# Kernel tuning notes

Hardware: AMD Instinct MI355X
Metric: run time of the kernel (lower is better)

The kernel has to match this reference:

```python
import jax, jax.numpy as jnp
import numpy as np

D_MODEL = 1024
N_HEAD = 16
D_HEAD = D_MODEL // N_HEAD


def setup_inputs() -> dict:
    key = jax.random.key(0)
    k1, k2, k3 = jax.random.split(key, 3)
    x = jax.random.normal(k1, (4, 1024, D_MODEL), dtype=jnp.float32)
    # torch Linear(d_model, 3*d_model, bias=False): weight [3*d_model, d_model], y = x @ W.T
    w_qkv = jax.random.normal(k2, (3 * D_MODEL, D_MODEL), dtype=jnp.float32) * (1.0 / np.sqrt(D_MODEL))
    w_out = jax.random.normal(k3, (D_MODEL, D_MODEL), dtype=jnp.float32) * (1.0 / np.sqrt(D_MODEL))
    return {"x": x, "w_qkv": w_qkv, "w_out": w_out}


def reference(x, w_qkv, w_out):
    B, T, C = x.shape
    qkv = x @ w_qkv.T                                   # [B,T,3C]
    qkv = qkv.reshape(B, T, 3, N_HEAD, D_HEAD)
    q = jnp.transpose(qkv[:, :, 0], (0, 2, 1, 3))       # [B,H,T,Dh]
    k = jnp.transpose(qkv[:, :, 1], (0, 2, 1, 3))
    v = jnp.transpose(qkv[:, :, 2], (0, 2, 1, 3))
    att = jnp.einsum('bhqd,bhkd->bhqk', q, k) / jnp.sqrt(jnp.float32(D_HEAD))
    causal = jnp.tril(jnp.ones((T, T), dtype=bool))
    att = jnp.where(causal[None, None], att, -jnp.inf)
    att = jax.nn.softmax(att, axis=-1)
    y = jnp.einsum('bhqk,bhkd->bhqd', att, v)           # [B,H,T,Dh]
    y = jnp.transpose(y, (0, 2, 1, 3)).reshape(B, T, C)
    return y @ w_out.T
```

## Files before the change

kernel.cpp:

```cpp
#include <hip/hip_runtime.h>
#include <hip/hip_bf16.h>
#include <stdint.h>

#define DM 1024
#define NH 16
#define DH 64
#define BB 4
#define TT 1024
#define MR (BB*TT)

typedef __attribute__((ext_vector_type(8))) short bf16x8;
typedef __attribute__((ext_vector_type(4))) float f32x4;

typedef unsigned int __attribute__((address_space(1))) uint_g;
typedef unsigned int __attribute__((address_space(3))) uint_l;

static __device__ __forceinline__ void gload_lds16(const void* g, void* l) {
  __builtin_amdgcn_global_load_lds((const uint_g*)g, (uint_l*)l, 16, 0, 0);
}

static __device__ __forceinline__ unsigned short f2bf(float f) {
  union { float f; unsigned int u; } v; v.f = f;
  unsigned int r = v.u + 0x7fffu + ((v.u >> 16) & 1u);
  return (unsigned short)(r >> 16);
}
static __device__ __forceinline__ unsigned short f2bf_fast(float f) {
  union { float f; unsigned int u; } v; v.f = f;
  return (unsigned short)((v.u + 0x8000u) >> 16);
}

__global__ __launch_bounds__(256) void k_cvt3(const float* __restrict__ x,
    const float* __restrict__ w1, const float* __restrict__ w2,
    unsigned short* __restrict__ xb, unsigned short* __restrict__ wqb,
    unsigned short* __restrict__ wob) {
  const int n1 = (MR * DM) / 4, n2 = (3 * DM * DM) / 4, n3 = (DM * DM) / 4;
  const int total = n1 + n2 + n3;
  for (int u = blockIdx.x * 256 + threadIdx.x; u < total; u += gridDim.x * 256) {
    const float* src; unsigned short* dst; int i;
    if (u < n1)           { src = x;  dst = xb;  i = u; }
    else if (u < n1 + n2) { src = w1; dst = wqb; i = u - n1; }
    else                  { src = w2; dst = wob; i = u - n1 - n2; }
    float4 v = reinterpret_cast<const float4*>(src)[i];
    ushort4 o;
    o.x = f2bf(v.x); o.y = f2bf(v.y); o.z = f2bf(v.z); o.w = f2bf(v.w);
    reinterpret_cast<ushort4*>(dst)[i] = o;
  }
}

template<int EPI>
__global__ __launch_bounds__(256) void k_gemm(
    const unsigned short* __restrict__ A, const unsigned short* __restrict__ Bw,
    float* __restrict__ Of, unsigned short* __restrict__ qb,
    unsigned short* __restrict__ kb, unsigned short* __restrict__ vtb,
    int N, int K, int tiles_n) {
  __shared__ unsigned short SH[2][2][128 * 32];
  int tid = threadIdx.x;
  int w = tid >> 6, l = tid & 63;
  int l15 = l & 15, k8 = l >> 4;
  int nwg = gridDim.x;
  int cpx = nwg >> 3;
  int wg = blockIdx.x;
  int swz = (wg & 7) * cpx + (wg >> 3);
  int tm = swz / tiles_n, tn = swz % tiles_n;
  int m0 = tm << 7, n0 = tn << 7;

  f32x4 acc[4][4];
  #pragma unroll
  for (int i = 0; i < 4; ++i)
    #pragma unroll
    for (int j = 0; j < 4; ++j) acc[i][j] = (f32x4){0.f, 0.f, 0.f, 0.f};

  int srow = (w << 4) + (l >> 2);
  int sch = l & 3;
  int mrb = ((w >> 1) << 6) + l15;
  int nrb = ((w & 1) << 6) + l15;

  auto stage = [&](int buf, int kk) {
    #pragma unroll
    for (int p = 0; p < 2; ++p) {
      int row = srow + (p << 6);
      int c = sch ^ ((row >> 1) & 3);
      int seg = w + (p << 2);
      gload_lds16(A + (size_t)(m0 + row) * K + kk + (c << 3), &SH[buf][0][seg << 9]);
      gload_lds16(Bw + (size_t)(n0 + row) * K + kk + (c << 3), &SH[buf][1][seg << 9]);
    }
  };

  stage(0, 0);
  __syncthreads();
  int cur = 0;
  for (int kk = 0; kk < K; kk += 32) {
    if (kk + 32 < K) stage(cur ^ 1, kk + 32);
    bf16x8 a[4], b[4];
    #pragma unroll
    for (int mf = 0; mf < 4; ++mf) {
      int row = mrb + (mf << 4);
      a[mf] = *(const bf16x8*)&SH[cur][0][(row << 5) + ((k8 ^ ((row >> 1) & 3)) << 3)];
    }
    #pragma unroll
    for (int nf = 0; nf < 4; ++nf) {
      int row = nrb + (nf << 4);
      b[nf] = *(const bf16x8*)&SH[cur][1][(row << 5) + ((k8 ^ ((row >> 1) & 3)) << 3)];
    }
    #pragma unroll
    for (int mf = 0; mf < 4; ++mf)
      #pragma unroll
      for (int nf = 0; nf < 4; ++nf)
        acc[mf][nf] = __builtin_amdgcn_mfma_f32_16x16x32_bf16(a[mf], b[nf], acc[mf][nf], 0, 0, 0);
    __syncthreads();
    cur ^= 1;
  }

  if (EPI == 1) {
    #pragma unroll
    for (int mf = 0; mf < 4; ++mf)
      #pragma unroll
      for (int nf = 0; nf < 4; ++nf) {
        int n = n0 + ((w & 1) << 6) + (nf << 4) + l15;
        int m_base = m0 + ((w >> 1) << 6) + (mf << 4) + (k8 << 2);
        #pragma unroll
        for (int r = 0; r < 4; ++r)
          Of[(size_t)(m_base + r) * N + n] = acc[mf][nf][r];
      }
    return;
  }

  int s = n0 >> 10;
  if (s < 2) {
    #pragma unroll
    for (int mf = 0; mf < 4; ++mf) {
      #pragma unroll
      for (int nf = 0; nf < 4; ++nf) {
        int n = n0 + ((w & 1) << 6) + (nf << 4) + l15;
        int rem = n & 1023;
        int h = rem >> 6, d = rem & 63;
        int m_base = m0 + ((w >> 1) << 6) + (mf << 4) + (k8 << 2);
        #pragma unroll
        for (int r = 0; r < 4; ++r) {
          int m = m_base + r;
          int bb = m >> 10, t = m & 1023;
          float v = acc[mf][nf][r];
          if (s == 0)
            qb[((size_t)(bb * NH + h) * TT + t) * DH + d] = f2bf(v * 0.125f);
          else
            kb[((size_t)(bb * NH + h) * TT + t) * DH + d] = f2bf(v);
        }
      }
    }
  } else {
    unsigned short* T = &SH[0][0][0];
    int bb = m0 >> 10, t0 = m0 & 1023;
    int myhalf = w & 1;
    #pragma unroll
    for (int half = 0; half < 2; ++half) {
      __syncthreads();
      if (myhalf == half) {
        #pragma unroll
        for (int nf = 0; nf < 4; ++nf) {
          int nloc = (nf << 4) + l15;
          #pragma unroll
          for (int mf = 0; mf < 4; ++mf) {
            int mloc = ((w >> 1) << 6) + (mf << 4) + (k8 << 2);
            #pragma unroll
            for (int r = 0; r < 4; ++r)
              T[nloc * 134 + mloc + r] = f2bf(acc[mf][nf][r]);
          }
        }
      }
      __syncthreads();
      {
        int d = tid >> 2, mseg = tid & 3;
        int n = n0 + (half << 6) + d;
        int h = (n & 1023) >> 6;
        size_t base = ((size_t)(bb * NH + h) * DH + d) * TT + t0 + (mseg << 5);
        #pragma unroll
        for (int i = 0; i < 4; ++i) {
          ushort4 v4 = *(const ushort4*)&T[d * 134 + (mseg << 5) + (i << 3)];
          ushort4 v4b = *(const ushort4*)&T[d * 134 + (mseg << 5) + (i << 3) + 4];
          *(ushort4*)&vtb[base + (i << 3)] = v4;
          *(ushort4*)&vtb[base + (i << 3) + 4] = v4b;
        }
      }
    }
  }
}

__global__ __launch_bounds__(256) void k_gemm1(
    const unsigned short* __restrict__ A, const unsigned short* __restrict__ Bw,
    float* __restrict__ Of, int N, int K) {
  __shared__ unsigned short At[2][64 * 32];
  __shared__ unsigned short Bt[2][128 * 32];
  int tid = threadIdx.x;
  int w = tid >> 6, l = tid & 63;
  int l15 = l & 15, k8 = l >> 4;
  int wg = blockIdx.x;
  int swz = (wg & 7) * 64 + (wg >> 3);
  int tm = swz >> 3, tn = swz & 7;
  int m0 = tm << 6, n0 = tn << 7;
  int wm = w >> 1, wn = w & 1;

  f32x4 acc[2][4];
  #pragma unroll
  for (int i = 0; i < 2; ++i)
    #pragma unroll
    for (int j = 0; j < 4; ++j) acc[i][j] = (f32x4){0.f, 0.f, 0.f, 0.f};

  int srl = l >> 2;
  int sch = l & 3;

  auto stage = [&](int buf, int kk) {
    {
      int row = (w << 4) + srl;
      int c = sch ^ ((row >> 1) & 3);
      gload_lds16(A + (size_t)(m0 + row) * K + kk + (c << 3), &At[buf][w << 9]);
    }
    #pragma unroll
    for (int p = 0; p < 2; ++p) {
      int seg = (w << 1) + p;
      int row = (seg << 4) + srl;
      int c = sch ^ ((row >> 1) & 3);
      gload_lds16(Bw + (size_t)(n0 + row) * K + kk + (c << 3), &Bt[buf][seg << 9]);
    }
  };

  stage(0, 0);
  __syncthreads();
  int cur = 0;
  for (int kk = 0; kk < K; kk += 32) {
    if (kk + 32 < K) stage(cur ^ 1, kk + 32);
    bf16x8 a[2], b[4];
    #pragma unroll
    for (int mf = 0; mf < 2; ++mf) {
      int row = (wm << 5) + (mf << 4) + l15;
      a[mf] = *(const bf16x8*)&At[cur][(row << 5) + ((k8 ^ ((row >> 1) & 3)) << 3)];
    }
    #pragma unroll
    for (int nf = 0; nf < 4; ++nf) {
      int row = (wn << 6) + (nf << 4) + l15;
      b[nf] = *(const bf16x8*)&Bt[cur][(row << 5) + ((k8 ^ ((row >> 1) & 3)) << 3)];
    }
    #pragma unroll
    for (int mf = 0; mf < 2; ++mf)
      #pragma unroll
      for (int nf = 0; nf < 4; ++nf)
        acc[mf][nf] = __builtin_amdgcn_mfma_f32_16x16x32_bf16(a[mf], b[nf], acc[mf][nf], 0, 0, 0);
    __syncthreads();
    cur ^= 1;
  }

  #pragma unroll
  for (int mf = 0; mf < 2; ++mf)
    #pragma unroll
    for (int nf = 0; nf < 4; ++nf) {
      int n = n0 + (wn << 6) + (nf << 4) + l15;
      int m_base = m0 + (wm << 5) + (mf << 4) + (k8 << 2);
      #pragma unroll
      for (int r = 0; r < 4; ++r)
        Of[(size_t)(m_base + r) * N + n] = acc[mf][nf][r];
    }
}

__global__ __launch_bounds__(512) void k_attn(
    const unsigned short* __restrict__ qb, const unsigned short* __restrict__ kb,
    const unsigned short* __restrict__ vtb, unsigned short* __restrict__ yb) {
  __shared__ unsigned short Kt[2][64 * 64];
  __shared__ unsigned short Vt[2][64 * 64];
  __shared__ unsigned short Pl[8][16][72];
  int tid = threadIdx.x, w = tid >> 6, l = tid & 63;
  int l15 = l & 15, k8 = l >> 4;
  int bh = blockIdx.x >> 3;
  int a = blockIdx.x & 7;
  int wlo = w & 3;
  int qb_w = (w < 4) ? ((a << 6) + (wlo << 4))
                     : ((TT - ((a + 1) << 6)) + (wlo << 4));
  const unsigned short* Kb = kb + (size_t)bh * TT * DH;
  const unsigned short* Vb = vtb + (size_t)bh * DH * TT;
  const unsigned short* Qb = qb + (size_t)bh * TT * DH;

  int qrow = qb_w + l15;
  bf16x8 qf[2];
  #pragma unroll
  for (int c = 0; c < 2; ++c)
    qf[c] = *(const bf16x8*)&Qb[(size_t)qrow * DH + (c << 5) + (k8 << 3)];

  f32x4 y[4];
  #pragma unroll
  for (int i = 0; i < 4; ++i) y[i] = (f32x4){0.f, 0.f, 0.f, 0.f};
  float mrow = -INFINITY, lrow = 0.f;

  int srow = l >> 3;
  int sch = l & 7;

  auto stage = [&](int buf, int j0) {
    int row = (w << 3) + srow;
    int c = sch ^ (row & 7);
    gload_lds16(Kb + (size_t)(j0 + row) * DH + (c << 3), &Kt[buf][(w << 3) << 6]);
    gload_lds16(Vb + (size_t)row * TT + j0 + (c << 3), &Vt[buf][(w << 3) << 6]);
  };

  const int ns = 16 - a;
  stage(0, 0);
  __syncthreads();
  int cur = 0;

  for (int t = 0; t < ns; ++t) {
    int j0 = t << 6;
    if (t + 1 < ns) stage(cur ^ 1, (t + 1) << 6);

    if (j0 <= qb_w + 15) {
      f32x4 s[4];
      #pragma unroll
      for (int f = 0; f < 4; ++f) s[f] = (f32x4){0.f, 0.f, 0.f, 0.f};
      __builtin_amdgcn_s_setprio(1);
      #pragma unroll
      for (int c = 0; c < 2; ++c) {
        #pragma unroll
        for (int f = 0; f < 4; ++f) {
          int row = (f << 4) + l15;
          bf16x8 ak = *(const bf16x8*)&Kt[cur][(row << 6) + ((((c << 2) + k8) ^ (row & 7)) << 3)];
          s[f] = __builtin_amdgcn_mfma_f32_16x16x32_bf16(ak, qf[c], s[f], 0, 0, 0);
        }
      }
      __builtin_amdgcn_s_setprio(0);

      if (j0 + 64 > qb_w) {
        #pragma unroll
        for (int f = 0; f < 4; ++f)
          #pragma unroll
          for (int r = 0; r < 4; ++r)
            if (j0 + (f << 4) + (k8 << 2) + r > qrow) s[f][r] = -INFINITY;
      }

      float pmax = -INFINITY;
      #pragma unroll
      for (int f = 0; f < 4; ++f)
        #pragma unroll
        for (int r = 0; r < 4; ++r) pmax = fmaxf(pmax, s[f][r]);
      pmax = fmaxf(pmax, __shfl_xor(pmax, 16, 64));
      pmax = fmaxf(pmax, __shfl_xor(pmax, 32, 64));

      bool skip = __all(pmax - mrow <= 8.0f);
      float mnew = skip ? mrow : fmaxf(mrow, pmax);
      float psum = 0.f;
      #pragma unroll
      for (int f = 0; f < 4; ++f)
        #pragma unroll
        for (int r = 0; r < 4; ++r) {
          float p = __expf(s[f][r] - mnew);
          s[f][r] = p;
          psum += p;
        }
      psum += __shfl_xor(psum, 16, 64);
      psum += __shfl_xor(psum, 32, 64);
      if (!skip) {
        float alpha = __expf(mrow - mnew);
        lrow *= alpha;
        #pragma unroll
        for (int mf = 0; mf < 4; ++mf) y[mf] *= alpha;
        mrow = mnew;
      }
      lrow += psum;

      #pragma unroll
      for (int f = 0; f < 4; ++f) {
        ushort4 pk;
        pk.x = f2bf_fast(s[f][0]); pk.y = f2bf_fast(s[f][1]);
        pk.z = f2bf_fast(s[f][2]); pk.w = f2bf_fast(s[f][3]);
        *(ushort4*)&Pl[w][l15][(f << 4) + (k8 << 2)] = pk;
      }
      asm volatile("s_waitcnt lgkmcnt(0)" ::: "memory");
      __builtin_amdgcn_sched_barrier(0);

      __builtin_amdgcn_s_setprio(1);
      #pragma unroll
      for (int c = 0; c < 2; ++c) {
        bf16x8 bp = *(const bf16x8*)&Pl[w][l15][(c << 5) + (k8 << 3)];
        #pragma unroll
        for (int mf = 0; mf < 4; ++mf) {
          int dr = (mf << 4) + l15;
          bf16x8 av = *(const bf16x8*)&Vt[cur][(dr << 6) + ((((c << 2) + k8) ^ (dr & 7)) << 3)];
          y[mf] = __builtin_amdgcn_mfma_f32_16x16x32_bf16(av, bp, y[mf], 0, 0, 0);
        }
      }
      __builtin_amdgcn_s_setprio(0);
    }

    __syncthreads();
    cur ^= 1;
  }

  float inv = 1.f / lrow;
  int bb = bh >> 4, h = bh & 15;
  #pragma unroll
  for (int mf = 0; mf < 4; ++mf) {
    ushort4 o;
    o.x = f2bf(y[mf][0] * inv);
    o.y = f2bf(y[mf][1] * inv);
    o.z = f2bf(y[mf][2] * inv);
    o.w = f2bf(y[mf][3] * inv);
    *(ushort4*)&yb[((size_t)(bb * TT + qrow) << 10) + (h << 6) + (mf << 4) + (k8 << 2)] = o;
  }
}

extern "C" void kernel_launch(void* const* d_in, const int* in_sizes, int n_in,
                              void* d_out, int out_size, void* d_ws, size_t ws_size,
                              hipStream_t stream) {
  const float* x    = (const float*)d_in[0];
  const float* wqkv = (const float*)d_in[1];
  const float* wout = (const float*)d_in[2];
  char* ws = (char*)d_ws;
  unsigned short* xb  = (unsigned short*)(ws + (size_t)0);
  unsigned short* wqb = (unsigned short*)(ws + ((size_t)8  << 20));
  unsigned short* wob = (unsigned short*)(ws + ((size_t)14 << 20));
  unsigned short* qbv = (unsigned short*)(ws + ((size_t)16 << 20));
  unsigned short* kbv = (unsigned short*)(ws + ((size_t)24 << 20));
  unsigned short* vtb = (unsigned short*)(ws + ((size_t)32 << 20));
  unsigned short* yb  = (unsigned short*)(ws + ((size_t)40 << 20));

  k_cvt3<<<2048, 256, 0, stream>>>(x, wqkv, wout, xb, wqb, wob);
  k_gemm<0><<<768, 256, 0, stream>>>(xb, wqb, nullptr, qbv, kbv, vtb, 3 * DM, DM, 24);
  k_attn<<<512, 512, 0, stream>>>(qbv, kbv, vtb, yb);
  k_gemm1<<<512, 256, 0, stream>>>(yb, wob, (float*)d_out, DM, DM);
}
```

Baseline: 94.80 us.

## Rewrite QKV GEMM as 256x256-tile 8-wave kernel with phased pipelining

Replaces the 128x128-tile, 4-wave QKV projection GEMM with a 256x256-tile, 512-thread kernel. It uses a 64-wide K step, explicit barrier-phased interleaving of global-to-LDS loads with MFMA groups, s_setprio around the MFMA bursts and manual vmcnt waits. Larger tiles raise arithmetic intensity and reduce global traffic per FLOP. The cost is only 192 workgroups, which is fewer than the CU count on the target, so part of the GPU may sit idle. Register pressure also goes up, with 32 accumulators plus the B fragments per thread. The V-transpose epilogue is adapted to the larger tile with 16-byte stores.

```diff
diff --git a/kernel.cpp b/kernel.cpp
--- a/kernel.cpp
+++ b/kernel.cpp
@@ -18,6 +18,8 @@
 static __device__ __forceinline__ void gload_lds16(const void* g, void* l) {
   __builtin_amdgcn_global_load_lds((const uint_g*)g, (uint_l*)l, 16, 0, 0);
 }
+
+static __device__ __forceinline__ void fence() { asm volatile("" ::: "memory"); }
 
 static __device__ __forceinline__ unsigned short f2bf(float f) {
   union { float f; unsigned int u; } v; v.f = f;
@@ -47,98 +49,124 @@
   }
 }
 
-template<int EPI>
-__global__ __launch_bounds__(256) void k_gemm(
+__global__ __launch_bounds__(512) void k_gemm8(
     const unsigned short* __restrict__ A, const unsigned short* __restrict__ Bw,
-    float* __restrict__ Of, unsigned short* __restrict__ qb,
-    unsigned short* __restrict__ kb, unsigned short* __restrict__ vtb,
-    int N, int K, int tiles_n) {
-  __shared__ unsigned short SH[2][2][128 * 32];
-  int tid = threadIdx.x;
-  int w = tid >> 6, l = tid & 63;
+    unsigned short* __restrict__ qb, unsigned short* __restrict__ kb,
+    unsigned short* __restrict__ vtb) {
+  const int K = DM, nt = K >> 6, ni = nt >> 1;
+  __shared__ unsigned short lds[2][2][16384];
+  int tid = threadIdx.x, w = tid >> 6, l = tid & 63;
   int l15 = l & 15, k8 = l >> 4;
-  int nwg = gridDim.x;
-  int cpx = nwg >> 3;
+  int wm = w >> 2, wn = w & 3;
   int wg = blockIdx.x;
-  int swz = (wg & 7) * cpx + (wg >> 3);
-  int tm = swz / tiles_n, tn = swz % tiles_n;
-  int m0 = tm << 7, n0 = tn << 7;
-
-  f32x4 acc[4][4];
-  #pragma unroll
-  for (int i = 0; i < 4; ++i)
+  int swz = (wg & 7) * 24 + (wg >> 3);
+  int tm = swz / 12, tn = swz % 12;
+  int m0 = tm << 8, n0 = tn << 8;
+
+  f32x4 acc[8][4];
+  #pragma unroll
+  for (int i = 0; i < 8; ++i)
     #pragma unroll
     for (int j = 0; j < 4; ++j) acc[i][j] = (f32x4){0.f, 0.f, 0.f, 0.f};
-
-  int srow = (w << 4) + (l >> 2);
-  int sch = l & 3;
-  int mrb = ((w >> 1) << 6) + l15;
-  int nrb = ((w & 1) << 6) + l15;
-
-  auto stage = [&](int buf, int kk) {
-    #pragma unroll
-    for (int p = 0; p < 2; ++p) {
-      int row = srow + (p << 6);
-      int c = sch ^ ((row >> 1) & 3);
-      int seg = w + (p << 2);
-      gload_lds16(A + (size_t)(m0 + row) * K + kk + (c << 3), &SH[buf][0][seg << 9]);
-      gload_lds16(Bw + (size_t)(n0 + row) * K + kk + (c << 3), &SH[buf][1][seg << 9]);
-    }
-  };
-
-  stage(0, 0);
-  __syncthreads();
-  int cur = 0;
-  for (int kk = 0; kk < K; kk += 32) {
-    if (kk + 32 < K) stage(cur ^ 1, kk + 32);
-    bf16x8 a[4], b[4];
-    #pragma unroll
-    for (int mf = 0; mf < 4; ++mf) {
-      int row = mrb + (mf << 4);
-      a[mf] = *(const bf16x8*)&SH[cur][0][(row << 5) + ((k8 ^ ((row >> 1) & 3)) << 3)];
-    }
-    #pragma unroll
-    for (int nf = 0; nf < 4; ++nf) {
-      int row = nrb + (nf << 4);
-      b[nf] = *(const bf16x8*)&SH[cur][1][(row << 5) + ((k8 ^ ((row >> 1) & 3)) << 3)];
-    }
-    #pragma unroll
-    for (int mf = 0; mf < 4; ++mf)
-      #pragma unroll
-      for (int nf = 0; nf < 4; ++nf)
-        acc[mf][nf] = __builtin_amdgcn_mfma_f32_16x16x32_bf16(a[mf], b[nf], acc[mf][nf], 0, 0, 0);
-    __syncthreads();
-    cur ^= 1;
-  }
-
-  if (EPI == 1) {
-    #pragma unroll
-    for (int mf = 0; mf < 4; ++mf)
+  bf16x8 b[4][2];
+
+  int sr = l >> 2;
+  int scc = (l & 3) ^ (((l >> 5) & 1) << 1);
+
+  auto stA = [&](int buf, int half, int t) {
+    int R = (half << 7) + (w << 4) + sr;
+    const unsigned short* src = A + (size_t)(m0 + R) * K + (t << 6);
+    #pragma unroll
+    for (int q2 = 0; q2 < 2; ++q2)
+      gload_lds16(src + (((q2 << 2) + scc) << 3),
+                  &lds[buf][0][(half << 13) + (w << 10) + (q2 << 9)]);
+  };
+  auto stB = [&](int buf, int half, int t) {
+    int R = (half << 7) + (w << 4) + sr;
+    const unsigned short* src = Bw + (size_t)(n0 + R) * K + (t << 6);
+    #pragma unroll
+    for (int q2 = 0; q2 < 2; ++q2)
+      gload_lds16(src + (((q2 << 2) + scc) << 3),
+                  &lds[buf][1][(half << 13) + (w << 10) + (q2 << 9)]);
+  };
+  auto ldA = [&](int buf, int mf, int ks) -> bf16x8 {
+    int off = (wm << 13) + (mf << 10) + (ks << 9) + (l15 << 5)
+            + ((k8 << 3) ^ ((l15 & 8) << 1));
+    return *(const bf16x8*)&lds[buf][0][off];
+  };
+  auto ldB = [&](int buf, int nf, int ks) -> bf16x8 {
+    int off = ((wn >> 1) << 13) + ((((wn & 1) << 2) + nf) << 10) + (ks << 9)
+            + (l15 << 5) + ((k8 << 3) ^ ((l15 & 8) << 1));
+    return *(const bf16x8*)&lds[buf][1][off];
+  };
+
+#define GPH(BUF, Q, LOADB, STAGE, TAIL)                                        \
+  {                                                                            \
+    if (LOADB) {                                                               \
+      _Pragma("unroll") for (int nf = 0; nf < 4; ++nf) {                       \
+        b[nf][0] = ldB(BUF, nf, 0);                                            \
+        b[nf][1] = ldB(BUF, nf, 1);                                            \
+      }                                                                        \
+    }                                                                          \
+    bf16x8 a00 = ldA(BUF, 2 * Q, 0);                                           \
+    bf16x8 a01 = ldA(BUF, 2 * Q, 1);                                           \
+    bf16x8 a10 = ldA(BUF, 2 * Q + 1, 0);                                       \
+    bf16x8 a11 = ldA(BUF, 2 * Q + 1, 1);                                       \
+    STAGE;                                                                     \
+    fence(); __builtin_amdgcn_s_barrier(); fence();                            \
+    asm volatile("s_waitcnt lgkmcnt(0)" ::: "memory");                         \
+    __builtin_amdgcn_sched_barrier(0);                                         \
+    __builtin_amdgcn_s_setprio(1);                                             \
+    _Pragma("unroll") for (int nf = 0; nf < 4; ++nf) {                         \
+      acc[2 * Q][nf]     = __builtin_amdgcn_mfma_f32_16x16x32_bf16(a00, b[nf][0], acc[2 * Q][nf], 0, 0, 0);     \
+      acc[2 * Q][nf]     = __builtin_amdgcn_mfma_f32_16x16x32_bf16(a01, b[nf][1], acc[2 * Q][nf], 0, 0, 0);     \
+      acc[2 * Q + 1][nf] = __builtin_amdgcn_mfma_f32_16x16x32_bf16(a10, b[nf][0], acc[2 * Q + 1][nf], 0, 0, 0); \
+      acc[2 * Q + 1][nf] = __builtin_amdgcn_mfma_f32_16x16x32_bf16(a11, b[nf][1], acc[2 * Q + 1][nf], 0, 0, 0); \
+    }                                                                          \
+    __builtin_amdgcn_s_setprio(0);                                             \
+    TAIL;                                                                      \
+    fence(); __builtin_amdgcn_s_barrier(); fence();                            \
+  }
+
+  stB(0, 0, 0); stB(0, 1, 0);
+  stA(0, 0, 0); stA(0, 1, 0);
+  stB(1, 0, 1); stB(1, 1, 1);
+  asm volatile("s_waitcnt vmcnt(4)" ::: "memory");
+  fence(); __builtin_amdgcn_s_barrier(); fence();
+
+  for (int i = 0; i < ni; ++i) {
+    int t0 = 2 * i, t1 = t0 + 1;
+    bool mid = (i + 1 < ni);
+    GPH(0, 0, true,  { stA(1, 0, t1); }, {});
+    GPH(0, 1, false, { stA(1, 1, t1); if (mid) stB(0, 0, t0 + 2); }, {});
+    GPH(0, 2, false, { if (mid) stB(0, 1, t0 + 2); }, {});
+    GPH(0, 3, false, {},
+        { if (mid) { asm volatile("s_waitcnt vmcnt(4)" ::: "memory"); }
+          else     { asm volatile("s_waitcnt vmcnt(0)" ::: "memory"); } });
+    GPH(1, 0, true,  { if (mid) stA(0, 0, t0 + 2); }, {});
+    GPH(1, 1, false, { if (mid) stA(0, 1, t0 + 2); }, {});
+    GPH(1, 2, false, { if (mid) stB(1, 0, t1 + 2); }, {});
+    GPH(1, 3, false, { if (mid) stB(1, 1, t1 + 2); },
+        { if (mid) { asm volatile("s_waitcnt vmcnt(4)" ::: "memory"); }
+          else     { asm volatile("s_waitcnt vmcnt(0)" ::: "memory"); } });
+  }
+#undef GPH
+
+  int s = n0 >> 10;
+  int bb = m0 >> 10, t0m = m0 & 1023;
+  if (s < 2) {
+    #pragma unroll
+    for (int mf = 0; mf < 8; ++mf) {
       #pragma unroll
       for (int nf = 0; nf < 4; ++nf) {
-        int n = n0 + ((w & 1) << 6) + (nf << 4) + l15;
-        int m_base = m0 + ((w >> 1) << 6) + (mf << 4) + (k8 << 2);
-        #pragma unroll
-        for (int r = 0; r < 4; ++r)
-          Of[(size_t)(m_base + r) * N + n] = acc[mf][nf][r];
-      }
-    return;
-  }
-
-  int s = n0 >> 10;
-  if (s < 2) {
-    #pragma unroll
-    for (int mf = 0; mf < 4; ++mf) {
-      #pragma unroll
-      for (int nf = 0; nf < 4; ++nf) {
-        int n = n0 + ((w & 1) << 6) + (nf << 4) + l15;
+        int n = n0 + (wn << 6) + (nf << 4) + l15;
         int rem = n & 1023;
         int h = rem >> 6, d = rem & 63;
-        int m_base = m0 + ((w >> 1) << 6) + (mf << 4) + (k8 << 2);
+        int m_base = m0 + (wm << 7) + (mf << 4) + (k8 << 2);
         #pragma unroll
         for (int r = 0; r < 4; ++r) {
           int m = m_base + r;
-          int bb = m >> 10, t = m & 1023;
+          int t = m & 1023;
           float v = acc[mf][nf][r];
           if (s == 0)
             qb[((size_t)(bb * NH + h) * TT + t) * DH + d] = f2bf(v * 0.125f);
@@ -148,37 +176,35 @@
       }
     }
   } else {
-    unsigned short* T = &SH[0][0][0];
-    int bb = m0 >> 10, t0 = m0 & 1023;
-    int myhalf = w & 1;
-    #pragma unroll
-    for (int half = 0; half < 2; ++half) {
+    unsigned short* T = &lds[0][0][0];
+    #pragma unroll
+    for (int qn = 0; qn < 4; ++qn) {
       __syncthreads();
-      if (myhalf == half) {
+      if (wn == qn) {
         #pragma unroll
         for (int nf = 0; nf < 4; ++nf) {
           int nloc = (nf << 4) + l15;
           #pragma unroll
-          for (int mf = 0; mf < 4; ++mf) {
-            int mloc = ((w >> 1) << 6) + (mf << 4) + (k8 << 2);
-            #pragma unroll
-            for (int r = 0; r < 4; ++r)
-              T[nloc * 134 + mloc + r] = f2bf(acc[mf][nf][r]);
+          for (int mf = 0; mf < 8; ++mf) {
+            int mrow = (wm << 7) + (mf << 4) + (k8 << 2);
+            ushort4 pk;
+            pk.x = f2bf(acc[mf][nf][0]); pk.y = f2bf(acc[mf][nf][1]);
+            pk.z = f2bf(acc[mf][nf][2]); pk.w = f2bf(acc[mf][nf][3]);
+            *(ushort4*)&T[nloc * 264 + mrow] = pk;
           }
         }
       }
       __syncthreads();
       {
-        int d = tid >> 2, mseg = tid & 3;
-        int n = n0 + (half << 6) + d;
-        int h = (n & 1023) >> 6;
-        size_t base = ((size_t)(bb * NH + h) * DH + d) * TT + t0 + (mseg << 5);
-        #pragma unroll
-        for (int i = 0; i < 4; ++i) {
-          ushort4 v4 = *(const ushort4*)&T[d * 134 + (mseg << 5) + (i << 3)];
-          ushort4 v4b = *(const ushort4*)&T[d * 134 + (mseg << 5) + (i << 3) + 4];
-          *(ushort4*)&vtb[base + (i << 3)] = v4;
-          *(ushort4*)&vtb[base + (i << 3) + 4] = v4b;
+        int d = tid >> 3, mseg = tid & 7;
+        int n = n0 + (qn << 6) + d;
+        int rem = n & 1023;
+        int h = rem >> 6;
+        size_t base = ((size_t)(bb * NH + h) * DH + d) * TT + t0m + (mseg << 5);
+        #pragma unroll
+        for (int j = 0; j < 4; ++j) {
+          bf16x8 v = *(const bf16x8*)&T[d * 264 + (mseg << 5) + (j << 3)];
+          *(bf16x8*)&vtb[base + (j << 3)] = v;
         }
       }
     }
@@ -418,7 +444,7 @@
   unsigned short* yb  = (unsigned short*)(ws + ((size_t)40 << 20));
 
   k_cvt3<<<2048, 256, 0, stream>>>(x, wqkv, wout, xb, wqb, wob);
-  k_gemm<0><<<768, 256, 0, stream>>>(xb, wqb, nullptr, qbv, kbv, vtb, 3 * DM, DM, 24);
+  k_gemm8<<<192, 512, 0, stream>>>(xb, wqb, qbv, kbv, vtb);
   k_attn<<<512, 512, 0, stream>>>(qbv, kbv, vtb, yb);
   k_gemm1<<<512, 256, 0, stream>>>(yb, wob, (float*)d_out, DM, DM);
 }
```

Result: no change. 95.13 us (+0.3%).
